# Kernel tuning notes

Measured on AMD Instinct MI355X. Metric: run time of the kernel, lower is better.

## Reference

```python
import jax, jax.numpy as jnp
import numpy as np

NUM_HEADS = 12


def setup_inputs() -> dict:
    key = jax.random.key(0)
    ks = jax.random.split(key, 6)
    B, F, P, C = 2, 8, 196, 768
    N = 1 + F * P
    s = 0.02
    return {
        "x": jax.random.normal(ks[0], (B, N, C), jnp.float32),
        "Wqkv": jax.random.normal(ks[1], (C, 3 * C), jnp.float32) * s,
        "Wq": jax.random.normal(ks[2], (C, C), jnp.float32) * s,
        "Wkv": jax.random.normal(ks[3], (C, 2 * C), jnp.float32) * s,
        "Wproj": jax.random.normal(ks[4], (C, C), jnp.float32) * s,
        "bproj": jnp.zeros((C,), jnp.float32),
        "seq_len": 196,
        "num_frames": 8,
    }


def reference(x, Wqkv, Wq, Wkv, Wproj, bproj, seq_len, num_frames):
    B, N, C = x.shape
    H = NUM_HEADS
    d = C // H
    scale = d ** -0.5
    F, P = num_frames, seq_len
    S = F * P  # N == 1 + S

    qkv = x @ Wqkv                                # [B, N, 3C]
    q, k, v = jnp.split(qkv, 3, axis=-1)
    def to_heads(t):  # [B, N, C] -> [B*H, N, d]
        return t.reshape(B, N, H, d).transpose(0, 2, 1, 3).reshape(B * H, N, d)
    q, k, v = to_heads(q), to_heads(k), to_heads(v)

    # --- cls token attends over everything ---
    cls_q = q[:, :1] * scale                      # [BH, 1, d]
    cls_attn = jax.nn.softmax(jnp.einsum('bid,bjd->bij', cls_q, k), axis=-1)
    cls_out = jnp.einsum('bij,bjd->bid', cls_attn, v)  # [BH, 1, d]
    cls_out = cls_out.reshape(B, H, d).reshape(B, 1, C)

    # --- per-frame spatial softmax ---
    q_, k_, v_ = q[:, 1:], k[:, 1:], v[:, 1:]     # [BH, S, d]
    qk = jnp.einsum('bqd,bkd->bqk', q_, k_).reshape(B * H, S, F, P)
    sp_attn = jax.nn.softmax(scale * qk, axis=-1)  # softmax over patches within frame
    v_f = v_.reshape(B * H, F, P, d)
    xt = jnp.einsum('bqfn,bfnd->bqfd', sp_attn, v_f)  # [BH, S, F, d]

    x4 = xt.reshape(B, H, S, F, d).transpose(0, 2, 3, 1, 4).reshape(B, S, F, C)

    # --- diagonal extraction: query frame g == key frame f ---
    x5 = x4.reshape(B, F, P, F, C)
    xd = jnp.diagonal(x5, axis1=1, axis2=3)       # [B, P, C, F]
    xd = xd.transpose(0, 3, 1, 2).reshape(B, S, C)

    # --- temporal trajectory attention ---
    q2 = (xd @ Wq).reshape(B, S, H, d).transpose(0, 2, 1, 3) * scale  # [B,H,S,d]
    kv2 = x4 @ Wkv                                # [B, S, F, 2C]
    k2 = kv2[..., :C].reshape(B, S, F, H, d).transpose(0, 3, 1, 2, 4)  # [B,H,S,F,d]
    attn2 = jax.nn.softmax(jnp.einsum('bhsd,bhsfd->bhsf', q2, k2), axis=-1)
    # use_original_code=True: aggregate the trajectory tensor x4 itself
    xr = x4.reshape(B, S, F, H, d).transpose(0, 3, 1, 2, 4)            # [B,H,S,F,d]
    out = jnp.einsum('bhsf,bhsfd->bhsd', attn2, xr)
    out = out.transpose(0, 2, 1, 3).reshape(B, S, C)

    out = jnp.concatenate([cls_out, out], axis=1) @ Wproj + bproj      # [B, N, C]
    return out, attn2
```

## Files before the change

### kernel.cpp

```cpp
#include <hip/hip_runtime.h>

namespace {
constexpr int kB = 2;
constexpr int kH = 12;
constexpr int kD = 64;
constexpr int kC = 768;
constexpr int kF = 8;
constexpr int kP = 196;
constexpr int kS = kF * kP;
constexpr int kN = 1 + kS;
constexpr int k3C = 3 * kC;
constexpr float kScale = 0.125f;
constexpr int kBH = kB * kH;
constexpr int kPpad = 224;
constexpr int kLpad = 1600;
constexpr int kBS = kB * kS;
}

typedef __attribute__((ext_vector_type(8))) short bf16x8;
typedef __attribute__((ext_vector_type(8))) unsigned short u16x8;
typedef __attribute__((ext_vector_type(4))) float f32x4;
typedef __attribute__((ext_vector_type(4))) unsigned int u32x4;

__device__ inline ushort f2bf(float x) {
  union { float f; unsigned u; } v{x};
  unsigned r = v.u + 0x7fff + ((v.u >> 16) & 1);
  return (ushort)(r >> 16);
}
__device__ inline float bf2f(ushort u) {
  union { unsigned u; float f; } v{(unsigned)u << 16};
  return v.f;
}

__device__ __forceinline__ void gload_lds16(const void* g, void* l) {
  __builtin_amdgcn_global_load_lds(
      (const __attribute__((address_space(1))) unsigned int*)g,
      (__attribute__((address_space(3))) unsigned int*)l, 16, 0, 0);
}

__device__ inline void storeC(float v, float* p) { *p = v; }
__device__ inline void storeC(float v, ushort* p) { *p = f2bf(v); }

template <typename OutT>
__global__ __launch_bounds__(256) void gemm_bf16(
    const ushort* __restrict__ A, const ushort* __restrict__ Bt,
    const float* __restrict__ bias, OutT* __restrict__ C,
    int M, int N, int K, int nbx) {
  const int nwg = gridDim.x;
  const int q = nwg >> 3, rr = nwg & 7;
  const int xcd = blockIdx.x & 7, loc = blockIdx.x >> 3;
  const int vid = ((xcd < rr) ? xcd * (q + 1) : rr * (q + 1) + (xcd - rr) * q) + loc;
  const int m0 = (vid / nbx) * 128, n0 = (vid % nbx) * 128;

  __shared__ __align__(16) ushort As[128 * 32];
  __shared__ __align__(16) ushort Bs[128 * 32];
  const int tid = threadIdx.x;
  const int r0 = tid >> 2, c0 = tid & 3;
  const int r1 = r0 + 64;
  const int sc0 = (c0 ^ ((r0 >> 1) & 3)) * 8;
  const int sc1 = (c0 ^ ((r1 >> 1) & 3)) * 8;
  const int ar0 = min(m0 + r0, M - 1), ar1 = min(m0 + r1, M - 1);
  const ushort* ga0 = A + (size_t)ar0 * K + sc0;
  const ushort* ga1 = A + (size_t)ar1 * K + sc1;
  const ushort* gb0 = Bt + (size_t)(n0 + r0) * K + sc0;
  const ushort* gb1 = Bt + (size_t)(n0 + r1) * K + sc1;
  const int w = tid >> 6;
  char* lA0 = (char*)As + w * 1024;
  char* lA1 = (char*)As + 4096 + w * 1024;
  char* lB0 = (char*)Bs + w * 1024;
  char* lB1 = (char*)Bs + 4096 + w * 1024;
  const int lane = tid & 63;
  const int lr = lane & 15, lg = lane >> 4;
  const int wr = w >> 1, wc = w & 1;
  f32x4 acc[4][4] = {};
  for (int kt = 0; kt < K; kt += 32) {
    gload_lds16(ga0 + kt, lA0);
    gload_lds16(ga1 + kt, lA1);
    gload_lds16(gb0 + kt, lB0);
    gload_lds16(gb1 + kt, lB1);
    __syncthreads();
    bf16x8 af[4], bfr[4];
#pragma unroll
    for (int m = 0; m < 4; ++m) {
      int row = wr * 64 + m * 16 + lr;
      int ch = lg ^ ((row >> 1) & 3);
      af[m] = *(const bf16x8*)(As + row * 32 + ch * 8);
    }
#pragma unroll
    for (int n = 0; n < 4; ++n) {
      int row = wc * 64 + n * 16 + lr;
      int ch = lg ^ ((row >> 1) & 3);
      bfr[n] = *(const bf16x8*)(Bs + row * 32 + ch * 8);
    }
#pragma unroll
    for (int m = 0; m < 4; ++m)
#pragma unroll
      for (int n = 0; n < 4; ++n)
        acc[m][n] =
            __builtin_amdgcn_mfma_f32_16x16x32_bf16(af[m], bfr[n], acc[m][n], 0, 0, 0);
    __syncthreads();
  }
#pragma unroll
  for (int m = 0; m < 4; ++m) {
#pragma unroll
    for (int r = 0; r < 4; ++r) {
      const int mg = m0 + wr * 64 + m * 16 + lg * 4 + r;
      if (mg < M) {
        OutT* crow = C + (size_t)mg * N + n0 + wc * 64 + lr;
#pragma unroll
        for (int n = 0; n < 4; ++n) {
          float v = acc[m][n][r];
          if (bias) v += bias[n0 + wc * 64 + n * 16 + lr];
          storeC(v, crow + n * 16);
        }
      }
    }
  }
}

__global__ __launch_bounds__(256) void gemm_qkv(
    const ushort* __restrict__ A, const ushort* __restrict__ Bt,
    ushort* __restrict__ qkvb, ushort* __restrict__ Qb,
    ushort* __restrict__ Kb, ushort* __restrict__ Vt) {
  constexpr int M = 3138, N = k3C, K = kC, nbx = 18;
  const int nwg = gridDim.x;
  const int q = nwg >> 3, rr = nwg & 7;
  const int xcd = blockIdx.x & 7, loc = blockIdx.x >> 3;
  const int vid = ((xcd < rr) ? xcd * (q + 1) : rr * (q + 1) + (xcd - rr) * q) + loc;
  const int m0 = (vid / nbx) * 128, n0 = (vid % nbx) * 128;

  __shared__ __align__(16) ushort As[128 * 32];
  __shared__ __align__(16) ushort Bs[128 * 32];
  const int tid = threadIdx.x;
  const int r0 = tid >> 2, c0 = tid & 3;
  const int r1 = r0 + 64;
  const int sc0 = (c0 ^ ((r0 >> 1) & 3)) * 8;
  const int sc1 = (c0 ^ ((r1 >> 1) & 3)) * 8;
  const int ar0 = min(m0 + r0, M - 1), ar1 = min(m0 + r1, M - 1);
  const ushort* ga0 = A + (size_t)ar0 * K + sc0;
  const ushort* ga1 = A + (size_t)ar1 * K + sc1;
  const ushort* gb0 = Bt + (size_t)(n0 + r0) * K + sc0;
  const ushort* gb1 = Bt + (size_t)(n0 + r1) * K + sc1;
  const int w = tid >> 6;
  char* lA0 = (char*)As + w * 1024;
  char* lA1 = (char*)As + 4096 + w * 1024;
  char* lB0 = (char*)Bs + w * 1024;
  char* lB1 = (char*)Bs + 4096 + w * 1024;
  const int lane = tid & 63;
  const int lr = lane & 15, lg = lane >> 4;
  const int wr = w >> 1, wc = w & 1;
  f32x4 acc[4][4] = {};
  for (int kt = 0; kt < K; kt += 32) {
    gload_lds16(ga0 + kt, lA0);
    gload_lds16(ga1 + kt, lA1);
    gload_lds16(gb0 + kt, lB0);
    gload_lds16(gb1 + kt, lB1);
    __syncthreads();
    bf16x8 af[4], bfr[4];
#pragma unroll
    for (int m = 0; m < 4; ++m) {
      int row = wr * 64 + m * 16 + lr;
      int ch = lg ^ ((row >> 1) & 3);
      af[m] = *(const bf16x8*)(As + row * 32 + ch * 8);
    }
#pragma unroll
    for (int n = 0; n < 4; ++n) {
      int row = wc * 64 + n * 16 + lr;
      int ch = lg ^ ((row >> 1) & 3);
      bfr[n] = *(const bf16x8*)(Bs + row * 32 + ch * 8);
    }
#pragma unroll
    for (int m = 0; m < 4; ++m)
#pragma unroll
      for (int n = 0; n < 4; ++n)
        acc[m][n] =
            __builtin_amdgcn_mfma_f32_16x16x32_bf16(af[m], bfr[n], acc[m][n], 0, 0, 0);
    __syncthreads();
  }
#pragma unroll
  for (int m = 0; m < 4; ++m) {
#pragma unroll
    for (int r = 0; r < 4; ++r) {
      const int mg = m0 + wr * 64 + m * 16 + lg * 4 + r;
      if (mg >= M) continue;
      const int b = (mg >= kN) ? 1 : 0;
      const int tok = mg - b * kN;
      ushort* qrow = qkvb + (size_t)mg * k3C + n0 + wc * 64 + lr;
#pragma unroll
      for (int n = 0; n < 4; ++n) {
        const int col = n0 + wc * 64 + n * 16 + lr;
        const float v = acc[m][n][r];
        const ushort bv = f2bf(v);
        qrow[n * 16] = bv;
        if (tok >= 1) {
          const int s = tok - 1;
          const int sec = col / kC;
          const int cj = col - sec * kC;
          const int h = cj >> 6, j = cj & 63;
          const int bh = b * kH + h;
          if (sec == 0) {
            Qb[((size_t)bh * kS + s) * kD + j] = f2bf(v * kScale);
          } else if (sec == 1) {
            Kb[((size_t)bh * kS + s) * kD + j] = bv;
          } else {
            const int fq = s / kP, nn = s - fq * kP;
            Vt[(((size_t)(bh * kF + fq)) * kD + j) * kPpad + nn] = bv;
          }
        }
      }
    }
  }
}

__global__ __launch_bounds__(256) void gemm_q2(
    const ushort* __restrict__ x4b, const ushort* __restrict__ Bt,
    ushort* __restrict__ C) {
  constexpr int M = kBS, N = kC, K = kC, nbx = 6;
  const int nwg = gridDim.x;
  const int q = nwg >> 3, rr = nwg & 7;
  const int xcd = blockIdx.x & 7, loc = blockIdx.x >> 3;
  const int vid = ((xcd < rr) ? xcd * (q + 1) : rr * (q + 1) + (xcd - rr) * q) + loc;
  const int m0 = (vid / nbx) * 128, n0 = (vid % nbx) * 128;

  __shared__ __align__(16) ushort As[128 * 32];
  __shared__ __align__(16) ushort Bs[128 * 32];
  const int tid = threadIdx.x;
  const int r0 = tid >> 2, c0 = tid & 3;
  const int r1 = r0 + 64;
  const int sc0 = (c0 ^ ((r0 >> 1) & 3)) * 8;
  const int sc1 = (c0 ^ ((r1 >> 1) & 3)) * 8;
  const int ar0 = min(m0 + r0, M - 1), ar1 = min(m0 + r1, M - 1);
  const int fq0 = (ar0 % kS) / kP, fq1 = (ar1 % kS) / kP;
  const ushort* ga0 = x4b + ((size_t)ar0 * kF + fq0) * kC + sc0;
  const ushort* ga1 = x4b + ((size_t)ar1 * kF + fq1) * kC + sc1;
  const ushort* gb0 = Bt + (size_t)(n0 + r0) * K + sc0;
  const ushort* gb1 = Bt + (size_t)(n0 + r1) * K + sc1;
  const int w = tid >> 6;
  char* lA0 = (char*)As + w * 1024;
  char* lA1 = (char*)As + 4096 + w * 1024;
  char* lB0 = (char*)Bs + w * 1024;
  char* lB1 = (char*)Bs + 4096 + w * 1024;
  const int lane = tid & 63;
  const int lr = lane & 15, lg = lane >> 4;
  const int wr = w >> 1, wc = w & 1;
  f32x4 acc[4][4] = {};
  for (int kt = 0; kt < K; kt += 32) {
    gload_lds16(ga0 + kt, lA0);
    gload_lds16(ga1 + kt, lA1);
    gload_lds16(gb0 + kt, lB0);
    gload_lds16(gb1 + kt, lB1);
    __syncthreads();
    bf16x8 af[4], bfr[4];
#pragma unroll
    for (int m = 0; m < 4; ++m) {
      int row = wr * 64 + m * 16 + lr;
      int ch = lg ^ ((row >> 1) & 3);
      af[m] = *(const bf16x8*)(As + row * 32 + ch * 8);
    }
#pragma unroll
    for (int n = 0; n < 4; ++n) {
      int row = wc * 64 + n * 16 + lr;
      int ch = lg ^ ((row >> 1) & 3);
      bfr[n] = *(const bf16x8*)(Bs + row * 32 + ch * 8);
    }
#pragma unroll
    for (int m = 0; m < 4; ++m)
#pragma unroll
      for (int n = 0; n < 4; ++n)
        acc[m][n] =
            __builtin_amdgcn_mfma_f32_16x16x32_bf16(af[m], bfr[n], acc[m][n], 0, 0, 0);
    __syncthreads();
  }
#pragma unroll
  for (int m = 0; m < 4; ++m) {
#pragma unroll
    for (int r = 0; r < 4; ++r) {
      const int mg = m0 + wr * 64 + m * 16 + lg * 4 + r;
      if (mg < M) {
        ushort* crow = C + (size_t)mg * N + n0 + wc * 64 + lr;
#pragma unroll
        for (int n = 0; n < 4; ++n) crow[n * 16] = f2bf(acc[m][n][r]);
      }
    }
  }
}

__global__ __launch_bounds__(256) void w2_gemm(
    const ushort* __restrict__ q2b, const ushort* __restrict__ Wkvb,
    ushort* __restrict__ w2b) {
  const int nwg = gridDim.x;
  const int q = nwg >> 3, rr = nwg & 7;
  const int xcd = blockIdx.x & 7, loc = blockIdx.x >> 3;
  const int vid = ((xcd < rr) ? xcd * (q + 1) : rr * (q + 1) + (xcd - rr) * q) + loc;
  const int h = vid / 150;
  const int rem = vid - h * 150;
  const int m0 = (rem / 6) * 128, n0 = (rem % 6) * 128;

  __shared__ __align__(16) ushort As[128 * 32];
  __shared__ __align__(16) ushort Bs[128 * 32];
  const int tid = threadIdx.x;
  const int r0 = tid >> 2, c0 = tid & 3;
  const int r1 = r0 + 64;
  const int sc0 = (c0 ^ ((r0 >> 1) & 3)) * 8;
  const int sc1 = (c0 ^ ((r1 >> 1) & 3)) * 8;
  const int ar0 = min(m0 + r0, kBS - 1), ar1 = min(m0 + r1, kBS - 1);
  const ushort* ga0 = q2b + (size_t)ar0 * kC + h * 64 + sc0;
  const ushort* ga1 = q2b + (size_t)ar1 * kC + h * 64 + sc1;
  const ushort* gb0 = Wkvb + (size_t)(n0 + r0) * kC + h * 64 + sc0;
  const ushort* gb1 = Wkvb + (size_t)(n0 + r1) * kC + h * 64 + sc1;
  const int w = tid >> 6;
  char* lA0 = (char*)As + w * 1024;
  char* lA1 = (char*)As + 4096 + w * 1024;
  char* lB0 = (char*)Bs + w * 1024;
  char* lB1 = (char*)Bs + 4096 + w * 1024;
  const int lane = tid & 63;
  const int lr = lane & 15, lg = lane >> 4;
  const int wr = w >> 1, wc = w & 1;
  f32x4 acc[4][4] = {};
#pragma unroll
  for (int kt = 0; kt < 64; kt += 32) {
    gload_lds16(ga0 + kt, lA0);
    gload_lds16(ga1 + kt, lA1);
    gload_lds16(gb0 + kt, lB0);
    gload_lds16(gb1 + kt, lB1);
    __syncthreads();
    bf16x8 af[4], bfr[4];
#pragma unroll
    for (int m = 0; m < 4; ++m) {
      int row = wr * 64 + m * 16 + lr;
      int ch = lg ^ ((row >> 1) & 3);
      af[m] = *(const bf16x8*)(As + row * 32 + ch * 8);
    }
#pragma unroll
    for (int n = 0; n < 4; ++n) {
      int row = wc * 64 + n * 16 + lr;
      int ch = lg ^ ((row >> 1) & 3);
      bfr[n] = *(const bf16x8*)(Bs + row * 32 + ch * 8);
    }
#pragma unroll
    for (int m = 0; m < 4; ++m)
#pragma unroll
      for (int n = 0; n < 4; ++n)
        acc[m][n] =
            __builtin_amdgcn_mfma_f32_16x16x32_bf16(af[m], bfr[n], acc[m][n], 0, 0, 0);
    __syncthreads();
  }
#pragma unroll
  for (int m = 0; m < 4; ++m) {
#pragma unroll
    for (int r = 0; r < 4; ++r) {
      const int mg = m0 + wr * 64 + m * 16 + lg * 4 + r;
      if (mg < kBS) {
        ushort* crow = w2b + (size_t)mg * (kH * kC) + h * kC + n0 + wc * 64 + lr;
#pragma unroll
        for (int n = 0; n < 4; ++n) crow[n * 16] = f2bf(acc[m][n][r]);
      }
    }
  }
}

__global__ void pack_x_k(const float* __restrict__ X, ushort* __restrict__ Xb,
                         int n4) {
  const int i = blockIdx.x * 256 + threadIdx.x;
  if (i >= n4) return;
  float4 v = ((const float4*)X)[i];
  ushort4 o = {f2bf(v.x), f2bf(v.y), f2bf(v.z), f2bf(v.w)};
  ((ushort4*)Xb)[i] = o;
}

__global__ __launch_bounds__(256) void pack_wt_k(const float* __restrict__ W,
                                                 ushort* __restrict__ Wt,
                                                 int ldw, float scale) {
  __shared__ float t[32][33];
  const int nb = blockIdx.x * 32;
  const int kb = blockIdx.y * 32;
  const int tx = threadIdx.x & 31, ty = threadIdx.x >> 5;
#pragma unroll
  for (int i = 0; i < 32; i += 8)
    t[ty + i][tx] = W[(size_t)(kb + ty + i) * ldw + nb + tx];
  __syncthreads();
#pragma unroll
  for (int i = 0; i < 32; i += 8)
    Wt[(size_t)(nb + ty + i) * 768 + kb + tx] = f2bf(t[tx][ty + i] * scale);
}

__global__ void pack_wkv_k(const float* __restrict__ Wkv,
                           ushort* __restrict__ Wkvb) {
  const int i = blockIdx.x * 256 + threadIdx.x;
  if (i >= 768 * 192) return;
  const int c = i / 192, j4 = i - c * 192;
  float4 v = *(const float4*)(Wkv + (size_t)c * 1536 + j4 * 4);
  ushort4 o = {f2bf(v.x), f2bf(v.y), f2bf(v.z), f2bf(v.w)};
  *(ushort4*)(Wkvb + (size_t)c * 768 + j4 * 4) = o;
}

__global__ __launch_bounds__(64) void sp_attn_mfma(
    const ushort* __restrict__ Qb, const ushort* __restrict__ Kb,
    const ushort* __restrict__ Vt, ushort* __restrict__ x4b) {
  const int lane = threadIdx.x;
  const int fbh = blockIdx.x;
  const int f = fbh / 24, bh = fbh % 24;
  const int tile = blockIdx.y;
  const int q0 = tile * 32;
  const int lr = lane & 15;
  const int lg = lane >> 4;

  const ushort* qrow = Qb + ((size_t)bh * kS + q0 + lr) * kD + lg * 8;
  const bf16x8 a00 = *(const bf16x8*)qrow;
  const bf16x8 a01 = *(const bf16x8*)(qrow + 32);
  const bf16x8 a10 = *(const bf16x8*)(qrow + 16 * kD);
  const bf16x8 a11 = *(const bf16x8*)(qrow + 16 * kD + 32);

  f32x4 s0[13], s1[13];
  const ushort* kbase = Kb + ((size_t)bh * kS + f * kP + lr) * kD + lg * 8;
#pragma unroll
  for (int nt = 0; nt < 13; ++nt) {
    const ushort* kr = kbase + (size_t)nt * 16 * kD;
    bf16x8 b0 = *(const bf16x8*)kr;
    bf16x8 b1 = *(const bf16x8*)(kr + 32);
    f32x4 acc0 = {0.f, 0.f, 0.f, 0.f}, acc1 = {0.f, 0.f, 0.f, 0.f};
    acc0 = __builtin_amdgcn_mfma_f32_16x16x32_bf16(b0, a00, acc0, 0, 0, 0);
    acc0 = __builtin_amdgcn_mfma_f32_16x16x32_bf16(b1, a01, acc0, 0, 0, 0);
    acc1 = __builtin_amdgcn_mfma_f32_16x16x32_bf16(b0, a10, acc1, 0, 0, 0);
    acc1 = __builtin_amdgcn_mfma_f32_16x16x32_bf16(b1, a11, acc1, 0, 0, 0);
    s0[nt] = acc0;
    s1[nt] = acc1;
  }
  if (lg >= 1) {
#pragma unroll
    for (int r = 0; r < 4; ++r) { s0[12][r] = -1e30f; s1[12][r] = -1e30f; }
  }

  float m0 = -1e30f, m1 = -1e30f;
#pragma unroll
  for (int nt = 0; nt < 13; ++nt)
#pragma unroll
    for (int r = 0; r < 4; ++r) {
      m0 = fmaxf(m0, s0[nt][r]);
      m1 = fmaxf(m1, s1[nt][r]);
    }
  m0 = fmaxf(m0, __shfl_xor(m0, 16));
  m0 = fmaxf(m0, __shfl_xor(m0, 32));
  m1 = fmaxf(m1, __shfl_xor(m1, 16));
  m1 = fmaxf(m1, __shfl_xor(m1, 32));

  float sum0 = 0.f, sum1 = 0.f;
  u32x4 breg0[7], breg1[7];
#pragma unroll
  for (int blk = 0; blk < 7; ++blk) {
    unsigned pk0[2][2], pk1[2][2];
#pragma unroll
    for (int t = 0; t < 2; ++t) {
      const int nt = blk * 2 + t;
      if (nt < 13) {
        float e0 = __expf(s0[nt][0] - m0), e1 = __expf(s0[nt][1] - m0);
        float e2 = __expf(s0[nt][2] - m0), e3 = __expf(s0[nt][3] - m0);
        sum0 += (e0 + e1) + (e2 + e3);
        pk0[t][0] = ((unsigned)f2bf(e1) << 16) | f2bf(e0);
        pk0[t][1] = ((unsigned)f2bf(e3) << 16) | f2bf(e2);
        float g0 = __expf(s1[nt][0] - m1), g1 = __expf(s1[nt][1] - m1);
        float g2 = __expf(s1[nt][2] - m1), g3 = __expf(s1[nt][3] - m1);
        sum1 += (g0 + g1) + (g2 + g3);
        pk1[t][0] = ((unsigned)f2bf(g1) << 16) | f2bf(g0);
        pk1[t][1] = ((unsigned)f2bf(g3) << 16) | f2bf(g2);
      } else {
        pk0[t][0] = 0; pk0[t][1] = 0;
        pk1[t][0] = 0; pk1[t][1] = 0;
      }
    }
#pragma unroll
    for (int j2 = 0; j2 < 4; ++j2) {
      const int srcLane = ((lg & 1) * 2 + (j2 >> 1)) * 16 + lr;
      unsigned t0 = (unsigned)__shfl((int)pk0[0][j2 & 1], srcLane);
      unsigned t1 = (unsigned)__shfl((int)pk0[1][j2 & 1], srcLane);
      breg0[blk][j2] = (lg < 2) ? t0 : t1;
      unsigned u0 = (unsigned)__shfl((int)pk1[0][j2 & 1], srcLane);
      unsigned u1 = (unsigned)__shfl((int)pk1[1][j2 & 1], srcLane);
      breg1[blk][j2] = (lg < 2) ? u0 : u1;
    }
  }
  sum0 += __shfl_xor(sum0, 16);
  sum0 += __shfl_xor(sum0, 32);
  sum1 += __shfl_xor(sum1, 16);
  sum1 += __shfl_xor(sum1, 32);
  const float inv0 = 1.f / sum0, inv1 = 1.f / sum1;

  const ushort* vbase = Vt + ((size_t)(bh * kF + f) * kD + lr) * kPpad + lg * 8;
  f32x4 o0[4] = {}, o1[4] = {};
#pragma unroll
  for (int nt2 = 0; nt2 < 4; ++nt2) {
    const ushort* vb = vbase + (size_t)nt2 * 16 * kPpad;
#pragma unroll
    for (int blk = 0; blk < 7; ++blk) {
      bf16x8 av = *(const bf16x8*)(vb + blk * 32);
      bf16x8 pb0 = __builtin_bit_cast(bf16x8, breg0[blk]);
      bf16x8 pb1 = __builtin_bit_cast(bf16x8, breg1[blk]);
      o0[nt2] = __builtin_amdgcn_mfma_f32_16x16x32_bf16(av, pb0, o0[nt2], 0, 0, 0);
      o1[nt2] = __builtin_amdgcn_mfma_f32_16x16x32_bf16(av, pb1, o1[nt2], 0, 0, 0);
    }
  }

  const int b = bh / kH, h = bh % kH;
  const size_t base0 =
      ((size_t)(b * kS + q0 + lr) * kF + f) * kC + h * kD + lg * 4;
#pragma unroll
  for (int nt2 = 0; nt2 < 4; ++nt2) {
    ushort4 v0, v1;
    v0.x = f2bf(o0[nt2][0] * inv0);
    v0.y = f2bf(o0[nt2][1] * inv0);
    v0.z = f2bf(o0[nt2][2] * inv0);
    v0.w = f2bf(o0[nt2][3] * inv0);
    *(ushort4*)(x4b + base0 + nt2 * 16) = v0;
    v1.x = f2bf(o1[nt2][0] * inv1);
    v1.y = f2bf(o1[nt2][1] * inv1);
    v1.z = f2bf(o1[nt2][2] * inv1);
    v1.w = f2bf(o1[nt2][3] * inv1);
    *(ushort4*)(x4b + base0 + (size_t)16 * kF * kC + nt2 * 16) = v1;
  }
}

__global__ __launch_bounds__(256) void cls_logits_k(const ushort* __restrict__ qkvb,
                                                    float* __restrict__ logits) {
  const int chunk = blockIdx.x, bh = blockIdx.y;
  const int b = bh / kH, h = bh % kH;
  const int g = threadIdx.x & 15, row = threadIdx.x >> 4;
  const size_t base = (size_t)b * kN * k3C;
  const ushort* qp = qkvb + base + h * kD + g * 4;
  const float q0 = bf2f(qp[0]) * kScale, q1 = bf2f(qp[1]) * kScale;
  const float q2 = bf2f(qp[2]) * kScale, q3 = bf2f(qp[3]) * kScale;
#pragma unroll
  for (int i = 0; i < 16; ++i) {
    const int n = chunk * 256 + i * 16 + row;
    if (n < kN) {
      ushort4 kv =
          *(const ushort4*)(qkvb + base + (size_t)n * k3C + kC + h * kD + g * 4);
      float p = q0 * bf2f(kv.x) + q1 * bf2f(kv.y) + q2 * bf2f(kv.z) +
                q3 * bf2f(kv.w);
#pragma unroll
      for (int o = 8; o; o >>= 1) p += __shfl_xor(p, o, 16);
      if (g == 0) logits[bh * kLpad + n] = p;
    }
  }
}

__global__ __launch_bounds__(256) void cls_softmax_k(const float* __restrict__ logits,
                                                     float* __restrict__ pbuf) {
  __shared__ float red[8];
  const int bh = blockIdx.x, tid = threadIdx.x;
  float m = -1e30f;
  for (int n = tid; n < kN; n += 256) m = fmaxf(m, logits[bh * kLpad + n]);
#pragma unroll
  for (int o = 32; o; o >>= 1) m = fmaxf(m, __shfl_xor(m, o));
  if ((tid & 63) == 0) red[tid >> 6] = m;
  __syncthreads();
  m = fmaxf(fmaxf(red[0], red[1]), fmaxf(red[2], red[3]));
  float sum = 0.f;
  for (int n = tid; n < kN; n += 256) sum += __expf(logits[bh * kLpad + n] - m);
#pragma unroll
  for (int o = 32; o; o >>= 1) sum += __shfl_xor(sum, o);
  if ((tid & 63) == 0) red[4 + (tid >> 6)] = sum;
  __syncthreads();
  const float inv = 1.f / (red[4] + red[5] + red[6] + red[7]);
  for (int n = tid; n < kN; n += 256)
    pbuf[bh * kLpad + n] = __expf(logits[bh * kLpad + n] - m) * inv;
}

__global__ __launch_bounds__(256) void cls_pv_k(const ushort* __restrict__ qkvb,
                                                const float* __restrict__ pbuf,
                                                float* __restrict__ partial) {
  __shared__ float pb[256];
  const int chunk = blockIdx.x, bh = blockIdx.y;
  const int b = bh / kH, h = bh % kH;
  const int j = threadIdx.x & 63, part = threadIdx.x >> 6;
  const size_t base = (size_t)b * kN * k3C + 2 * kC + h * kD + j;
  float acc = 0.f;
#pragma unroll 4
  for (int i = 0; i < 64; ++i) {
    const int n = chunk * 256 + i * 4 + part;
    if (n < kN)
      acc = fmaf(pbuf[bh * kLpad + n], bf2f(qkvb[base + (size_t)n * k3C]), acc);
  }
  pb[threadIdx.x] = acc;
  __syncthreads();
  if (part == 0)
    partial[((size_t)bh * 7 + chunk) * kD + j] =
        pb[j] + pb[64 + j] + pb[128 + j] + pb[192 + j];
}

__global__ void cls_red_k(const float* __restrict__ partial,
                          ushort* __restrict__ xin_b) {
  const int bh = blockIdx.x, j = threadIdx.x;
  const int b = bh / kH, h = bh % kH;
  float s = 0.f;
#pragma unroll
  for (int c = 0; c < 7; ++c) s += partial[((size_t)bh * 7 + c) * kD + j];
  xin_b[(size_t)(b * kN) * kC + h * kD + j] = f2bf(s);
}

__global__ __launch_bounds__(256) void attn2_fused(
    const ushort* __restrict__ x4b, const ushort* __restrict__ w2b,
    ushort* __restrict__ xin_b, float* __restrict__ attn2out) {
  __shared__ __align__(16) ushort x4s[kF * kC];
  __shared__ __align__(16) ushort w2s[kH * kC];
  const int bs = blockIdx.x;
  const int b = bs / kS, s = bs - b * kS;
  const int tid = threadIdx.x;
  {
    const ulonglong2* src = (const ulonglong2*)(x4b + (size_t)bs * kF * kC);
    ulonglong2* dst = (ulonglong2*)x4s;
    for (int i = tid; i < kF * kC / 8; i += 256) dst[i] = src[i];
    const ulonglong2* srcw = (const ulonglong2*)(w2b + (size_t)bs * kH * kC);
    ulonglong2* dstw = (ulonglong2*)w2s;
    for (int i = tid; i < kH * kC / 8; i += 256) dstw[i] = srcw[i];
  }
  __syncthreads();
  const int w = tid >> 6, lane = tid & 63;
#pragma unroll
  for (int hh = 0; hh < 3; ++hh) {
    const int h = w * 3 + hh;
    float part[kF] = {};
#pragma unroll
    for (int i = 0; i < 3; ++i) {
      const int c = lane * 4 + i * 256;
      ushort4 wv = *(const ushort4*)&w2s[h * kC + c];
      const float w0 = bf2f(wv.x), w1 = bf2f(wv.y);
      const float w2v = bf2f(wv.z), w3 = bf2f(wv.w);
#pragma unroll
      for (int f = 0; f < kF; ++f) {
        ushort4 xv = *(const ushort4*)&x4s[f * kC + c];
        part[f] += bf2f(xv.x) * w0 + bf2f(xv.y) * w1 + bf2f(xv.z) * w2v +
                   bf2f(xv.w) * w3;
      }
    }
    float l[kF];
#pragma unroll
    for (int f = 0; f < kF; ++f) {
      float p = part[f];
#pragma unroll
      for (int o = 32; o; o >>= 1) p += __shfl_xor(p, o);
      l[f] = p;
    }
    float m = l[0];
#pragma unroll
    for (int f = 1; f < kF; ++f) m = fmaxf(m, l[f]);
    float sum = 0.f;
#pragma unroll
    for (int f = 0; f < kF; ++f) {
      l[f] = __expf(l[f] - m);
      sum += l[f];
    }
    const float inv = 1.f / sum;
    float pv = 0.f;
#pragma unroll
    for (int f = 0; f < kF; ++f) pv = (lane == f) ? l[f] : pv;
    if (lane < kF)
      attn2out[((size_t)(b * kH + h) * kS + s) * kF + lane] = pv * inv;
    float o = 0.f;
#pragma unroll
    for (int f = 0; f < kF; ++f)
      o = fmaf(l[f] * inv, bf2f(x4s[f * kC + h * kD + lane]), o);
    xin_b[(size_t)(b * kN + 1 + s) * kC + h * kD + lane] = f2bf(o);
  }
}

extern "C" void kernel_launch(void* const* d_in, const int* in_sizes, int n_in,
                              void* d_out, int out_size, void* d_ws,
                              size_t ws_size, hipStream_t stream) {
  const float* x = (const float*)d_in[0];
  const float* Wqkv = (const float*)d_in[1];
  const float* Wq = (const float*)d_in[2];
  const float* Wkv = (const float*)d_in[3];
  const float* Wproj = (const float*)d_in[4];
  const float* bproj = (const float*)d_in[5];

  char* p = (char*)d_ws;
  ushort* qkvb = (ushort*)p;         p += (size_t)3138 * 2304 * 2;
  ushort* w2b = (ushort*)p;          p += (size_t)kBS * kH * kC * 2;
  ushort* q2b = (ushort*)p;          p += (size_t)kBS * kC * 2;
  ushort* x4b = (ushort*)p;          p += (size_t)25088 * 768 * 2;
  ushort* xin_b = (ushort*)p;        p += (size_t)3138 * 768 * 2;
  ushort* xb = (ushort*)p;           p += (size_t)3138 * 768 * 2;
  ushort* Wqkv_t = (ushort*)p;       p += (size_t)2304 * 768 * 2;
  ushort* Wq_t = (ushort*)p;         p += (size_t)768 * 768 * 2;
  ushort* Wkvb = (ushort*)p;         p += (size_t)768 * 768 * 2;
  ushort* Wproj_t = (ushort*)p;      p += (size_t)768 * 768 * 2;
  ushort* Qb = (ushort*)p;           p += (size_t)kBH * kS * kD * 2;
  ushort* Kb = (ushort*)p;           p += ((size_t)kBH * kS + 16) * kD * 2;
  ushort* Vt = (ushort*)p;           p += (size_t)kBH * kF * kD * kPpad * 2;
  float* clsL = (float*)p;           p += (size_t)kBH * kLpad * 4;
  float* clsP = (float*)p;           p += (size_t)kBH * kLpad * 4;
  float* clsPart = (float*)p;

  float* out = (float*)d_out;
  float* attn2 = out + (size_t)kB * kN * kC;

  pack_x_k<<<(3138 * 768 / 4 + 255) / 256, 256, 0, stream>>>(x, xb, 3138 * 768 / 4);
  pack_wt_k<<<dim3(72, 24), 256, 0, stream>>>(Wqkv, Wqkv_t, 2304, 1.f);
  pack_wt_k<<<dim3(24, 24), 256, 0, stream>>>(Wq, Wq_t, 768, kScale);
  pack_wkv_k<<<(768 * 192 + 255) / 256, 256, 0, stream>>>(Wkv, Wkvb);
  pack_wt_k<<<dim3(24, 24), 256, 0, stream>>>(Wproj, Wproj_t, 768, 1.f);
  gemm_qkv<<<18 * 25, 256, 0, stream>>>(xb, Wqkv_t, qkvb, Qb, Kb, Vt);
  cls_logits_k<<<dim3(7, 24), 256, 0, stream>>>(qkvb, clsL);
  cls_softmax_k<<<24, 256, 0, stream>>>(clsL, clsP);
  cls_pv_k<<<dim3(7, 24), 256, 0, stream>>>(qkvb, clsP, clsPart);
  cls_red_k<<<24, 64, 0, stream>>>(clsPart, xin_b);
  sp_attn_mfma<<<dim3(192, 49), 64, 0, stream>>>(Qb, Kb, Vt, x4b);
  gemm_q2<<<6 * 25, 256, 0, stream>>>(x4b, Wq_t, q2b);
  w2_gemm<<<1800, 256, 0, stream>>>(q2b, Wkvb, w2b);
  attn2_fused<<<kBS, 256, 0, stream>>>(x4b, w2b, xin_b, attn2);
  gemm_bf16<float><<<6 * 25, 256, 0, stream>>>(xin_b, Wproj_t, bproj, out, 3138,
                                               768, 768, 6);
}
```

Measured before the change: 253.6 us.

## Merge pack kernels, split V transpose out of QKV GEMM, batch attention waves

Folds the five input/weight packing launches into one kernel that dispatches on block index. The scattered V-transpose store moves out of the QKV GEMM epilogue into a separate pack_vt_k kernel, which also writes zeros into the padded columns. Spatial attention now runs four 64-lane waves per 256-thread block instead of one wave per block, and raises wave priority around the MFMA loops with s_setprio. In exchange it adds an extra launch and a second read of V from qkvb, and the early return for tile>=49 leaves some waves idle.

Result: no change. 255.0 us (+0.6%).

```diff
diff --git a/kernel.cpp b/kernel.cpp
--- a/kernel.cpp
+++ b/kernel.cpp
@@ -121,7 +121,7 @@
 __global__ __launch_bounds__(256) void gemm_qkv(
     const ushort* __restrict__ A, const ushort* __restrict__ Bt,
     ushort* __restrict__ qkvb, ushort* __restrict__ Qb,
-    ushort* __restrict__ Kb, ushort* __restrict__ Vt) {
+    ushort* __restrict__ Kb) {
   constexpr int M = 3138, N = k3C, K = kC, nbx = 18;
   const int nwg = gridDim.x;
   const int q = nwg >> 3, rr = nwg & 7;
@@ -202,9 +202,6 @@
             Qb[((size_t)bh * kS + s) * kD + j] = f2bf(v * kScale);
           } else if (sec == 1) {
             Kb[((size_t)bh * kS + s) * kD + j] = bv;
-          } else {
-            const int fq = s / kP, nn = s - fq * kP;
-            Vt[(((size_t)(bh * kF + fq)) * kD + j) * kPpad + nn] = bv;
           }
         }
       }
@@ -359,48 +356,81 @@
   }
 }
 
-__global__ void pack_x_k(const float* __restrict__ X, ushort* __restrict__ Xb,
-                         int n4) {
-  const int i = blockIdx.x * 256 + threadIdx.x;
-  if (i >= n4) return;
-  float4 v = ((const float4*)X)[i];
-  ushort4 o = {f2bf(v.x), f2bf(v.y), f2bf(v.z), f2bf(v.w)};
-  ((ushort4*)Xb)[i] = o;
-}
-
-__global__ __launch_bounds__(256) void pack_wt_k(const float* __restrict__ W,
-                                                 ushort* __restrict__ Wt,
-                                                 int ldw, float scale) {
+__global__ __launch_bounds__(256) void pack_all_k(
+    const float* __restrict__ x, const float* __restrict__ Wqkv,
+    const float* __restrict__ Wq, const float* __restrict__ Wproj,
+    const float* __restrict__ Wkv, ushort* __restrict__ xb,
+    ushort* __restrict__ Wqkv_t, ushort* __restrict__ Wq_t,
+    ushort* __restrict__ Wproj_t, ushort* __restrict__ Wkvb) {
   __shared__ float t[32][33];
-  const int nb = blockIdx.x * 32;
-  const int kb = blockIdx.y * 32;
-  const int tx = threadIdx.x & 31, ty = threadIdx.x >> 5;
-#pragma unroll
-  for (int i = 0; i < 32; i += 8)
-    t[ty + i][tx] = W[(size_t)(kb + ty + i) * ldw + nb + tx];
-  __syncthreads();
-#pragma unroll
-  for (int i = 0; i < 32; i += 8)
-    Wt[(size_t)(nb + ty + i) * 768 + kb + tx] = f2bf(t[tx][ty + i] * scale);
-}
-
-__global__ void pack_wkv_k(const float* __restrict__ Wkv,
-                           ushort* __restrict__ Wkvb) {
-  const int i = blockIdx.x * 256 + threadIdx.x;
-  if (i >= 768 * 192) return;
+  int bid = blockIdx.x;
+  if (bid < 2354) {
+    const int i = bid * 256 + threadIdx.x;
+    if (i < 3138 * 768 / 4) {
+      float4 v = ((const float4*)x)[i];
+      ushort4 o = {f2bf(v.x), f2bf(v.y), f2bf(v.z), f2bf(v.w)};
+      ((ushort4*)xb)[i] = o;
+    }
+    return;
+  }
+  bid -= 2354;
+  if (bid < 2880) {
+    const float* W;
+    ushort* Wt;
+    int ldw, nbw;
+    float scale;
+    if (bid < 1728) {
+      W = Wqkv; Wt = Wqkv_t; ldw = 2304; nbw = 72; scale = 1.f;
+    } else if (bid < 2304) {
+      bid -= 1728;
+      W = Wq; Wt = Wq_t; ldw = 768; nbw = 24; scale = kScale;
+    } else {
+      bid -= 2304;
+      W = Wproj; Wt = Wproj_t; ldw = 768; nbw = 24; scale = 1.f;
+    }
+    const int nb = (bid % nbw) * 32, kb = (bid / nbw) * 32;
+    const int tx = threadIdx.x & 31, ty = threadIdx.x >> 5;
+#pragma unroll
+    for (int i = 0; i < 32; i += 8)
+      t[ty + i][tx] = W[(size_t)(kb + ty + i) * ldw + nb + tx];
+    __syncthreads();
+#pragma unroll
+    for (int i = 0; i < 32; i += 8)
+      Wt[(size_t)(nb + ty + i) * 768 + kb + tx] = f2bf(t[tx][ty + i] * scale);
+    return;
+  }
+  bid -= 2880;
+  const int i = bid * 256 + threadIdx.x;
   const int c = i / 192, j4 = i - c * 192;
   float4 v = *(const float4*)(Wkv + (size_t)c * 1536 + j4 * 4);
   ushort4 o = {f2bf(v.x), f2bf(v.y), f2bf(v.z), f2bf(v.w)};
   *(ushort4*)(Wkvb + (size_t)c * 768 + j4 * 4) = o;
 }
 
-__global__ __launch_bounds__(64) void sp_attn_mfma(
+__global__ void pack_vt_k(const ushort* __restrict__ qkvb,
+                          ushort* __restrict__ Vt) {
+  const int idx = blockIdx.x * 256 + threadIdx.x;
+  if (idx >= kBH * kF * kD * kPpad) return;
+  const int n = idx % kPpad;
+  const int j = (idx / kPpad) & 63;
+  const int f = (idx / (kPpad * kD)) & 7;
+  const int bh = idx / (kPpad * kD * kF);
+  const int b = bh / kH, h = bh % kH;
+  ushort v = 0;
+  if (n < kP)
+    v = qkvb[(size_t)(b * kN + 1 + f * kP + n) * k3C + 2 * kC + h * kD + j];
+  Vt[idx] = v;
+}
+
+__global__ __launch_bounds__(256) void sp_attn_mfma(
     const ushort* __restrict__ Qb, const ushort* __restrict__ Kb,
     const ushort* __restrict__ Vt, ushort* __restrict__ x4b) {
-  const int lane = threadIdx.x;
+  const int w = threadIdx.x >> 6;
+  const int lane = threadIdx.x & 63;
   const int fbh = blockIdx.x;
   const int f = fbh / 24, bh = fbh % 24;
-  const int tile = blockIdx.y;
+  const int tile = blockIdx.y * 4 + w;
+  if (tile >= 49) return;
   const int q0 = tile * 32;
   const int lr = lane & 15;
   const int lg = lane >> 4;
@@ -413,6 +443,7 @@
 
   f32x4 s0[13], s1[13];
   const ushort* kbase = Kb + ((size_t)bh * kS + f * kP + lr) * kD + lg * 8;
+  __builtin_amdgcn_s_setprio(1);
 #pragma unroll
   for (int nt = 0; nt < 13; ++nt) {
     const ushort* kr = kbase + (size_t)nt * 16 * kD;
@@ -426,6 +457,7 @@
     s0[nt] = acc0;
     s1[nt] = acc1;
   }
+  __builtin_amdgcn_s_setprio(0);
   if (lg >= 1) {
 #pragma unroll
     for (int r = 0; r < 4; ++r) { s0[12][r] = -1e30f; s1[12][r] = -1e30f; }
@@ -487,6 +519,7 @@
 
   const ushort* vbase = Vt + ((size_t)(bh * kF + f) * kD + lr) * kPpad + lg * 8;
   f32x4 o0[4] = {}, o1[4] = {};
+  __builtin_amdgcn_s_setprio(1);
 #pragma unroll
   for (int nt2 = 0; nt2 < 4; ++nt2) {
     const ushort* vb = vbase + (size_t)nt2 * 16 * kPpad;
@@ -499,6 +532,7 @@
       o1[nt2] = __builtin_amdgcn_mfma_f32_16x16x32_bf16(av, pb1, o1[nt2], 0, 0, 0);
     }
   }
+  __builtin_amdgcn_s_setprio(0);
 
   const int b = bh / kH, h = bh % kH;
   const size_t base0 =
@@ -694,17 +728,15 @@
   float* out = (float*)d_out;
   float* attn2 = out + (size_t)kB * kN * kC;
 
-  pack_x_k<<<(3138 * 768 / 4 + 255) / 256, 256, 0, stream>>>(x, xb, 3138 * 768 / 4);
-  pack_wt_k<<<dim3(72, 24), 256, 0, stream>>>(Wqkv, Wqkv_t, 2304, 1.f);
-  pack_wt_k<<<dim3(24, 24), 256, 0, stream>>>(Wq, Wq_t, 768, kScale);
-  pack_wkv_k<<<(768 * 192 + 255) / 256, 256, 0, stream>>>(Wkv, Wkvb);
-  pack_wt_k<<<dim3(24, 24), 256, 0, stream>>>(Wproj, Wproj_t, 768, 1.f);
-  gemm_qkv<<<18 * 25, 256, 0, stream>>>(xb, Wqkv_t, qkvb, Qb, Kb, Vt);
+  pack_all_k<<<5810, 256, 0, stream>>>(x, Wqkv, Wq, Wproj, Wkv, xb, Wqkv_t,
+                                       Wq_t, Wproj_t, Wkvb);
+  gemm_qkv<<<18 * 25, 256, 0, stream>>>(xb, Wqkv_t, qkvb, Qb, Kb);
+  pack_vt_k<<<(kBH * kF * kD * kPpad + 255) / 256, 256, 0, stream>>>(qkvb, Vt);
   cls_logits_k<<<dim3(7, 24), 256, 0, stream>>>(qkvb, clsL);
   cls_softmax_k<<<24, 256, 0, stream>>>(clsL, clsP);
   cls_pv_k<<<dim3(7, 24), 256, 0, stream>>>(qkvb, clsP, clsPart);
   cls_red_k<<<24, 64, 0, stream>>>(clsPart, xin_b);
-  sp_attn_mfma<<<dim3(192, 49), 64, 0, stream>>>(Qb, Kb, Vt, x4b);
+  sp_attn_mfma<<<dim3(192, 13), 256, 0, stream>>>(Qb, Kb, Vt, x4b);
   gemm_q2<<<6 * 25, 256, 0, stream>>>(x4b, Wq_t, q2b);
   w2_gemm<<<1800, 256, 0, stream>>>(q2b, Wkvb, w2b);
   attn2_fused<<<kBS, 256, 0, stream>>>(x4b, w2b, xin_b, attn2);
```
